# Kernel optimization log

Measured on AMD Instinct MI355X. Metric: run time of the kernel, lower is better.

Reference implementation:

```python
import jax, jax.numpy as jnp
import numpy as np

N = 50000
E = 800000
IN_DIM = 256
HID = 256
LAT = 64
H1 = 4
H2 = 4
O1 = HID // H1  # 64 per-head out of conv1
NEG_SLOPE = 0.2


def setup_inputs() -> dict:
    key = jax.random.key(0)
    ks = jax.random.split(key, 12)
    x = jax.random.normal(ks[0], (N, IN_DIM), dtype=jnp.float32)
    edge_index = jax.random.randint(ks[1], (2, E), 0, N, dtype=jnp.int64)
    g = lambda k, shape: jax.random.normal(k, shape, dtype=jnp.float32) * (1.0 / np.sqrt(shape[-1]))
    W1 = g(ks[2], (IN_DIM, H1 * O1))
    a_src1 = g(ks[3], (H1, O1))
    a_dst1 = g(ks[4], (H1, O1))
    b1 = jnp.zeros((H1 * O1,), dtype=jnp.float32)
    W2 = g(ks[5], (HID, H2 * LAT))
    a_src2 = g(ks[6], (H2, LAT))
    a_dst2 = g(ks[7], (H2, LAT))
    b2 = jnp.zeros((LAT,), dtype=jnp.float32)
    return {"x": x, "edge_index": edge_index, "W1": W1, "a_src1": a_src1,
            "a_dst1": a_dst1, "b1": b1, "W2": W2, "a_src2": a_src2,
            "a_dst2": a_dst2, "b2": b2}


def _gat_conv(x, src, dst, W, a_src, a_dst, bias, concat):
    # src/dst already include self-loops. x: (N, F_in)
    n, heads, out = x.shape[0], a_src.shape[0], a_src.shape[1]
    h = (x @ W).reshape(n, heads, out)                      # (N,H,O)
    al_src = jnp.einsum('nho,ho->nh', h, a_src)             # (N,H)
    al_dst = jnp.einsum('nho,ho->nh', h, a_dst)
    e = al_src[src] + al_dst[dst]                           # (Et,H)
    e = jnp.where(e > 0, e, NEG_SLOPE * e)                  # LeakyReLU(0.2)
    # softmax over incoming edges of each dst node
    m = jax.ops.segment_max(e, dst, num_segments=n)         # (N,H)
    p = jnp.exp(e - m[dst])
    denom = jax.ops.segment_sum(p, dst, num_segments=n)     # (N,H)
    alpha = p / denom[dst]                                  # (Et,H)
    msg = h[src] * alpha[:, :, None]                        # (Et,H,O)
    out_n = jax.ops.segment_sum(msg, dst, num_segments=n)   # (N,H,O)
    if concat:
        out_n = out_n.reshape(n, heads * out)
    else:
        out_n = out_n.mean(axis=1)
    return out_n + bias


def reference(x, edge_index, W1, a_src1, a_dst1, b1, W2, a_src2, a_dst2, b2):
    src, dst = edge_index[0], edge_index[1]
    # add self-loops (PyG GATConv default)
    loops = jnp.arange(N, dtype=edge_index.dtype)
    src_sl = jnp.concatenate([src, loops])
    dst_sl = jnp.concatenate([dst, loops])
    h = _gat_conv(x, src_sl, dst_sl, W1, a_src1, a_dst1, b1, concat=True)
    h = jax.nn.elu(h)
    z = _gat_conv(h, src_sl, dst_sl, W2, a_src2, a_dst2, b2, concat=False)
    # DotDecoder on original edge_index
    logits = jnp.einsum('ed,ed->e', z[src], z[dst])
    return logits
```

## Files before the change

kernel.cpp:

```cpp
#include <hip/hip_runtime.h>
#include <math.h>

#define N_NODES 50000
#define E_EDGES 800000
#define DIM 256
#define HEADS 4
#define HO 64
#define NEG_SLOPE 0.2f
#define SCAN_NBLK ((N_NODES + 255) / 256)

typedef __attribute__((ext_vector_type(8))) short bf16x8;
typedef __attribute__((ext_vector_type(4))) float f32x4;
typedef __attribute__((ext_vector_type(2))) float f32x2;

static __device__ inline ushort f2bf(float f) {
  union { float f; unsigned u; } v; v.f = f;
  unsigned r = (v.u + 0x7fff + ((v.u >> 16) & 1)) >> 16;
  return (ushort)r;
}
static __device__ inline float bf2f(ushort h) {
  union { unsigned u; float f; } v; v.u = ((unsigned)h) << 16;
  return v.f;
}

__global__ __launch_bounds__(256) void cvt_T2(const float* __restrict__ W1,
                                              const float* __restrict__ W2,
                                              ushort* __restrict__ bt1,
                                              ushort* __restrict__ bt2) {
  int gidx = blockIdx.x * 256 + threadIdx.x;
  const float* W = (gidx < DIM * DIM) ? W1 : W2;
  ushort* bt = (gidx < DIM * DIM) ? bt1 : bt2;
  int idx = gidx & (DIM * DIM - 1);
  int k = idx >> 8, n = idx & 255;
  bt[n * 256 + k] = f2bf(W[idx]);
}

#define GBM 128
#define GBK 32
#define LDK 40

template <bool AF32>
__global__ __launch_bounds__(256) void gemm_mfma(const void* __restrict__ Av,
                                                 const ushort* __restrict__ Bt,
                                                 ushort* __restrict__ Cbf, int M) {
  __shared__ __align__(16) ushort As[GBM][LDK];
  __shared__ __align__(16) ushort Bs[GBM][LDK];
  const int tid = threadIdx.x;
  const int lane = tid & 63;
  const int wave = tid >> 6;
  const int row0 = blockIdx.x * GBM;
  const int col0 = blockIdx.y * GBM;
  const int wm = (wave & 1) * 64;
  const int wn = (wave >> 1) * 64;
  const int rA = lane & 15;
  const int kb = (lane >> 4) * 8;

  f32x4 acc[4][4] = {};

  for (int k0 = 0; k0 < DIM; k0 += GBK) {
    if constexpr (AF32) {
      const float* A = (const float*)Av;
#pragma unroll
      for (int qq = 0; qq < 4; ++qq) {
        int q = tid + qq * 256;
        int r = q >> 3, c = q & 7;
        int grow = row0 + r;
        float4 v = make_float4(0.f, 0.f, 0.f, 0.f);
        if (grow < M) v = *(const float4*)&A[(size_t)grow * DIM + k0 + c * 4];
        ushort4 h;
        h.x = f2bf(v.x); h.y = f2bf(v.y); h.z = f2bf(v.z); h.w = f2bf(v.w);
        *(ushort4*)&As[r][c * 4] = h;
      }
    } else {
      const ushort* A = (const ushort*)Av;
#pragma unroll
      for (int qq = 0; qq < 2; ++qq) {
        int q = tid + qq * 256;
        int r = q >> 2, c = q & 3;
        int grow = row0 + r;
        bf16x8 v = {};
        if (grow < M) v = *(const bf16x8*)&A[(size_t)grow * DIM + k0 + c * 8];
        *(bf16x8*)&As[r][c * 8] = v;
      }
    }
#pragma unroll
    for (int qq = 0; qq < 2; ++qq) {
      int q = tid + qq * 256;
      int r = q >> 2, c = q & 3;
      *(bf16x8*)&Bs[r][c * 8] = *(const bf16x8*)&Bt[(size_t)(col0 + r) * DIM + k0 + c * 8];
    }
    __syncthreads();

    bf16x8 af[4], bfr[4];
#pragma unroll
    for (int mi = 0; mi < 4; ++mi) af[mi] = *(const bf16x8*)&As[wm + mi * 16 + rA][kb];
#pragma unroll
    for (int ni = 0; ni < 4; ++ni) bfr[ni] = *(const bf16x8*)&Bs[wn + ni * 16 + rA][kb];
#pragma unroll
    for (int mi = 0; mi < 4; ++mi)
#pragma unroll
      for (int ni = 0; ni < 4; ++ni)
        acc[mi][ni] = __builtin_amdgcn_mfma_f32_16x16x32_bf16(af[mi], bfr[ni], acc[mi][ni], 0, 0, 0);
    __syncthreads();
  }

#pragma unroll
  for (int mi = 0; mi < 4; ++mi) {
    int rbase = row0 + wm + mi * 16 + (lane >> 4) * 4;
#pragma unroll
    for (int ni = 0; ni < 4; ++ni) {
      int col = col0 + wn + ni * 16 + (lane & 15);
#pragma unroll
      for (int r = 0; r < 4; ++r) {
        int row = rbase + r;
        if (row < M) Cbf[(size_t)row * DIM + col] = f2bf(acc[mi][ni][r]);
      }
    }
  }
}

__global__ __launch_bounds__(256) void attn_logits(const ushort* __restrict__ h,
                                                   const float* __restrict__ a_src,
                                                   const float* __restrict__ a_dst,
                                                   float* __restrict__ al_s,
                                                   float* __restrict__ al_d) {
  int gid = blockIdx.x * blockDim.x + threadIdx.x;
  int node = gid >> 6;
  int lane = threadIdx.x & 63;
  if (node >= N_NODES) return;
  ushort4 hv = *(const ushort4*)&h[(size_t)node * DIM + lane * 4];
  float4 as = *(const float4*)&a_src[lane * 4];
  float4 ad = *(const float4*)&a_dst[lane * 4];
  float h0 = bf2f(hv.x), h1 = bf2f(hv.y), h2 = bf2f(hv.z), h3 = bf2f(hv.w);
  float s = h0 * as.x + h1 * as.y + h2 * as.z + h3 * as.w;
  float d = h0 * ad.x + h1 * ad.y + h2 * ad.z + h3 * ad.w;
#pragma unroll
  for (int off = 8; off >= 1; off >>= 1) {
    s += __shfl_xor(s, off, 64);
    d += __shfl_xor(d, off, 64);
  }
  if ((lane & 15) == 0) {
    int head = lane >> 4;
    al_s[node * HEADS + head] = s;
    al_d[node * HEADS + head] = d;
  }
}

__global__ __launch_bounds__(256) void histo(const int* __restrict__ dst, int* __restrict__ deg) {
  int e = blockIdx.x * blockDim.x + threadIdx.x;
  if (e < E_EDGES) atomicAdd(&deg[dst[e]], 1);
}

__global__ __launch_bounds__(256) void scan1(const int* __restrict__ deg,
                                             int* __restrict__ excl,
                                             int* __restrict__ blockSums) {
  __shared__ int tmp[256];
  int i = blockIdx.x * 256 + threadIdx.x;
  int v = (i < N_NODES) ? deg[i] : 0;
  tmp[threadIdx.x] = v;
  __syncthreads();
  for (int off = 1; off < 256; off <<= 1) {
    int t = (threadIdx.x >= off) ? tmp[threadIdx.x - off] : 0;
    __syncthreads();
    tmp[threadIdx.x] += t;
    __syncthreads();
  }
  int incl = tmp[threadIdx.x];
  if (i < N_NODES) excl[i] = incl - v;
  if (threadIdx.x == 255) blockSums[blockIdx.x] = incl;
}

__global__ __launch_bounds__(256) void scan2(int* __restrict__ blockSums) {
  __shared__ int tmp[256];
  int i = threadIdx.x;
  int v = (i < SCAN_NBLK) ? blockSums[i] : 0;
  tmp[i] = v;
  __syncthreads();
  for (int off = 1; off < 256; off <<= 1) {
    int t = (i >= off) ? tmp[i - off] : 0;
    __syncthreads();
    tmp[i] += t;
    __syncthreads();
  }
  if (i < SCAN_NBLK) blockSums[i] = tmp[i] - v;
}

__global__ __launch_bounds__(256) void scan3(int* __restrict__ excl,
                                             const int* __restrict__ blockSums,
                                             int* __restrict__ cursor) {
  int i = blockIdx.x * 256 + threadIdx.x;
  if (i < N_NODES) {
    int r = excl[i] + blockSums[blockIdx.x];
    excl[i] = r;
    cursor[i] = r;
  }
}

__global__ __launch_bounds__(256) void scatter(const int* __restrict__ src,
                                               const int* __restrict__ dst,
                                               int* __restrict__ cursor,
                                               int* __restrict__ csr_src) {
  int e = blockIdx.x * blockDim.x + threadIdx.x;
  if (e >= E_EDGES) return;
  int pos = atomicAdd(&cursor[dst[e]], 1);
  csr_src[pos] = src[e];
}

#define AGG_BODY(S)                                                         \
  {                                                                         \
    float e0 = als[(S) * HEADS + head] + aldv;                              \
    e0 = e0 > 0.f ? e0 : NEG_SLOPE * e0;                                    \
    float p = __expf(e0);                                                   \
    bf16x8 hv = *(const bf16x8*)&hbf[(size_t)(S) * DIM + c0];               \
    den += p;                                                               \
    const uint* uu = (const uint*)&hv;                                      \
    f32x2 pp = {p, p};                                                      \
    _Pragma("unroll")                                                       \
    for (int q = 0; q < 4; ++q) {                                           \
      f32x2 hh;                                                             \
      hh.x = __uint_as_float(uu[q] << 16);                                  \
      hh.y = __uint_as_float(uu[q] & 0xffff0000u);                          \
      acc2[q] += pp * hh;                                                   \
    }                                                                       \
  }

#define AGG_LOOP                                                            \
  int rs = rowptr[node];                                                    \
  int deg = ((node < N_NODES - 1) ? rowptr[node + 1] : E_EDGES) - rs;       \
  float aldv = ald[node * HEADS + head];                                    \
  float den = 0.f;                                                          \
  f32x2 acc2[4] = {};                                                       \
  int total = deg + 1;                                                      \
  int it = half;                                                            \
  for (; it + 4 < total; it += 6) {                                         \
    int s0 = csr_src[rs + it];                                              \
    int s1 = csr_src[rs + it + 2];                                          \
    int s2 = (it + 4 < deg) ? csr_src[rs + it + 4] : node;                  \
    AGG_BODY(s0)                                                            \
    AGG_BODY(s1)                                                            \
    AGG_BODY(s2)                                                            \
  }                                                                         \
  for (; it < total; it += 2) {                                             \
    int s0 = (it < deg) ? csr_src[rs + it] : node;                          \
    AGG_BODY(s0)                                                            \
  }                                                                         \
  den += __shfl_xor(den, 32, 64);                                           \
  float accs[8];                                                            \
  _Pragma("unroll")                                                         \
  for (int q = 0; q < 4; ++q) {                                             \
    accs[2 * q] = acc2[q].x + __shfl_xor(acc2[q].x, 32, 64);                \
    accs[2 * q + 1] = acc2[q].y + __shfl_xor(acc2[q].y, 32, 64);            \
  }

__global__ __launch_bounds__(256) void agg1(const int* __restrict__ rowptr,
                                            const int* __restrict__ csr_src,
                                            const ushort* __restrict__ hbf,
                                            const float* __restrict__ als,
                                            const float* __restrict__ ald,
                                            const float* __restrict__ bias,
                                            ushort* __restrict__ x2) {
  int gid = blockIdx.x * blockDim.x + threadIdx.x;
  int node = gid >> 6;
  if (node >= N_NODES) return;
  int lane = threadIdx.x & 63;
  int li = lane & 31, half = lane >> 5;
  int head = li >> 3;
  int c0 = li * 8;
  AGG_LOOP
  if (half == 0) {
    float inv = 1.f / den;
    ushort4 o0, o1;
    float r[8];
#pragma unroll
    for (int j = 0; j < 8; ++j) {
      r[j] = accs[j] * inv + bias[c0 + j];
      r[j] = r[j] > 0.f ? r[j] : expm1f(r[j]);
    }
    o0.x = f2bf(r[0]); o0.y = f2bf(r[1]); o0.z = f2bf(r[2]); o0.w = f2bf(r[3]);
    o1.x = f2bf(r[4]); o1.y = f2bf(r[5]); o1.z = f2bf(r[6]); o1.w = f2bf(r[7]);
    *(ushort4*)&x2[(size_t)node * DIM + c0] = o0;
    *(ushort4*)&x2[(size_t)node * DIM + c0 + 4] = o1;
  }
}

__global__ __launch_bounds__(256) void agg2(const int* __restrict__ rowptr,
                                            const int* __restrict__ csr_src,
                                            const ushort* __restrict__ hbf,
                                            const float* __restrict__ als,
                                            const float* __restrict__ ald,
                                            const float* __restrict__ b2,
                                            float* __restrict__ z) {
  int gid = blockIdx.x * blockDim.x + threadIdx.x;
  int node = gid >> 6;
  if (node >= N_NODES) return;
  int lane = threadIdx.x & 63;
  int li = lane & 31, half = lane >> 5;
  int head = li >> 3;
  int c0 = li * 8;
  AGG_LOOP
  float inv = 1.f / den;
  float r[8];
#pragma unroll
  for (int j = 0; j < 8; ++j) {
    r[j] = accs[j] * inv;
    r[j] += __shfl_xor(r[j], 8, 64);
    r[j] += __shfl_xor(r[j], 16, 64);
  }
  if (lane < 8) {
    int zc = li * 8;
    float4 v0 = make_float4(r[0] * 0.25f + b2[zc + 0], r[1] * 0.25f + b2[zc + 1],
                            r[2] * 0.25f + b2[zc + 2], r[3] * 0.25f + b2[zc + 3]);
    float4 v1 = make_float4(r[4] * 0.25f + b2[zc + 4], r[5] * 0.25f + b2[zc + 5],
                            r[6] * 0.25f + b2[zc + 6], r[7] * 0.25f + b2[zc + 7]);
    *(float4*)&z[(size_t)node * HO + zc] = v0;
    *(float4*)&z[(size_t)node * HO + zc + 4] = v1;
  }
}

__global__ __launch_bounds__(256) void decoder(const int* __restrict__ src,
                                               const int* __restrict__ dst,
                                               const float* __restrict__ z,
                                               float* __restrict__ out) {
  long long gid = (long long)blockIdx.x * blockDim.x + threadIdx.x;
  int e = (int)(gid >> 4);
  if (e >= E_EDGES) return;
  int l = threadIdx.x & 15;
  int s = src[e];
  int d = dst[e];
  float4 a = *(const float4*)&z[(size_t)s * HO + l * 4];
  float4 b = *(const float4*)&z[(size_t)d * HO + l * 4];
  float v = a.x * b.x + a.y * b.y + a.z * b.z + a.w * b.w;
#pragma unroll
  for (int off = 8; off >= 1; off >>= 1) v += __shfl_xor(v, off, 64);
  if (l == 0) out[e] = v;
}

extern "C" void kernel_launch(void* const* d_in, const int* in_sizes, int n_in,
                              void* d_out, int out_size, void* d_ws, size_t ws_size,
                              hipStream_t stream) {
  const float* x      = (const float*)d_in[0];
  const int*   ei     = (const int*)d_in[1];
  const float* W1     = (const float*)d_in[2];
  const float* a_src1 = (const float*)d_in[3];
  const float* a_dst1 = (const float*)d_in[4];
  const float* b1     = (const float*)d_in[5];
  const float* W2     = (const float*)d_in[6];
  const float* a_src2 = (const float*)d_in[7];
  const float* a_dst2 = (const float*)d_in[8];
  const float* b2     = (const float*)d_in[9];
  const int* src = ei;
  const int* dst = ei + E_EDGES;
  float* logits = (float*)d_out;

  float* zlat = (float*)d_ws;
  float* als1 = zlat + (size_t)N_NODES * HO;
  float* ald1 = als1 + N_NODES * HEADS;
  float* als2 = ald1 + N_NODES * HEADS;
  float* ald2 = als2 + N_NODES * HEADS;
  int* deg      = (int*)(ald2 + N_NODES * HEADS);
  int* rowptr   = deg + N_NODES;
  int* cursor   = rowptr + N_NODES;
  int* blockSums= cursor + N_NODES;
  int* csr_src  = blockSums + 256;
  ushort* hbf   = (ushort*)(csr_src + E_EDGES);
  ushort* x2bf  = hbf + (size_t)N_NODES * DIM;
  ushort* bt1   = x2bf + (size_t)N_NODES * DIM;
  ushort* bt2   = bt1 + DIM * DIM;

  dim3 blk(256);
  dim3 gemmGrid((N_NODES + GBM - 1) / GBM, DIM / GBM);
  int nodeBlocks = (N_NODES * 64 + 255) / 256;
  int edgeThreadBlocks = (E_EDGES + 255) / 256;
  int decBlocks  = (int)(((long long)E_EDGES * 16 + 255) / 256);

  hipMemsetAsync(deg, 0, N_NODES * sizeof(int), stream);
  hipLaunchKernelGGL(histo, dim3(edgeThreadBlocks), blk, 0, stream, dst, deg);
  hipLaunchKernelGGL(scan1, dim3(SCAN_NBLK), blk, 0, stream, deg, rowptr, blockSums);
  hipLaunchKernelGGL(scan2, dim3(1), blk, 0, stream, blockSums);
  hipLaunchKernelGGL(scan3, dim3(SCAN_NBLK), blk, 0, stream, rowptr, blockSums, cursor);
  hipLaunchKernelGGL(scatter, dim3(edgeThreadBlocks), blk, 0, stream, src, dst, cursor, csr_src);

  hipLaunchKernelGGL(cvt_T2, dim3(2 * DIM * DIM / 256), blk, 0, stream, W1, W2, bt1, bt2);

  gemm_mfma<true><<<gemmGrid, blk, 0, stream>>>((const void*)x, bt1, hbf, N_NODES);
  hipLaunchKernelGGL(attn_logits, dim3(nodeBlocks), blk, 0, stream, hbf, a_src1, a_dst1, als1, ald1);
  hipLaunchKernelGGL(agg1, dim3(nodeBlocks), blk, 0, stream, rowptr, csr_src, hbf, als1, ald1, b1, x2bf);

  gemm_mfma<false><<<gemmGrid, blk, 0, stream>>>((const void*)x2bf, bt2, hbf, N_NODES);
  hipLaunchKernelGGL(attn_logits, dim3(nodeBlocks), blk, 0, stream, hbf, a_src2, a_dst2, als2, ald2);
  hipLaunchKernelGGL(agg2, dim3(nodeBlocks), blk, 0, stream, rowptr, csr_src, hbf, als2, ald2, b2, zlat);

  hipLaunchKernelGGL(decoder, dim3(decBlocks), blk, 0, stream, src, dst, zlat, logits);
}
```

Baseline: 378.3 us.

## Fold attention logit projections into GEMM via precomputed W·a columns

Precomputes W·a_src and W·a_dst per head as extra bf16 weight rows, so the GEMM blocks in column tile zero compute the attention logits with extra MFMAs. This removes the two attn_logits kernels, which re-read the full bf16 h matrix. In exchange, the logits are now computed from bf16-rounded folded weights rather than from rounded h, which changes the rounding slightly. The blockIdx.y==0 blocks also carry extra MFMA work, which unbalances the GEMM grid a little.

```diff
diff --git a/kernel.cpp b/kernel.cpp
--- a/kernel.cpp
+++ b/kernel.cpp
@@ -8,6 +8,7 @@
 #define HO 64
 #define NEG_SLOPE 0.2f
 #define SCAN_NBLK ((N_NODES + 255) / 256)
+#define BT_ROWS 272
 
 typedef __attribute__((ext_vector_type(8))) short bf16x8;
 typedef __attribute__((ext_vector_type(4))) float f32x4;
@@ -23,16 +24,42 @@
   return v.f;
 }
 
-__global__ __launch_bounds__(256) void cvt_T2(const float* __restrict__ W1,
-                                              const float* __restrict__ W2,
-                                              ushort* __restrict__ bt1,
-                                              ushort* __restrict__ bt2) {
-  int gidx = blockIdx.x * 256 + threadIdx.x;
-  const float* W = (gidx < DIM * DIM) ? W1 : W2;
-  ushort* bt = (gidx < DIM * DIM) ? bt1 : bt2;
-  int idx = gidx & (DIM * DIM - 1);
-  int k = idx >> 8, n = idx & 255;
-  bt[n * 256 + k] = f2bf(W[idx]);
+__global__ __launch_bounds__(256) void prep_weights(const float* __restrict__ W1,
+                                                    const float* __restrict__ W2,
+                                                    const float* __restrict__ as1,
+                                                    const float* __restrict__ ad1,
+                                                    const float* __restrict__ as2,
+                                                    const float* __restrict__ ad2,
+                                                    ushort* __restrict__ bt1,
+                                                    ushort* __restrict__ bt2) {
+  int b = blockIdx.x;
+  int tid = threadIdx.x;
+  if (b < 512) {
+    const float* W = (b < 256) ? W1 : W2;
+    ushort* bt = (b < 256) ? bt1 : bt2;
+    int idx = ((b & 255) << 8) | tid;
+    int k = idx >> 8, n = idx & 255;
+    bt[n * 256 + k] = f2bf(W[idx]);
+  } else {
+    int k = tid;
+    for (int l = 0; l < 2; ++l) {
+      const float* W = l ? W2 : W1;
+      const float* as = l ? as2 : as1;
+      const float* ad = l ? ad2 : ad1;
+      ushort* bt = l ? bt2 : bt1;
+      for (int h = 0; h < HEADS; ++h) {
+        float s = 0.f, d = 0.f;
+        for (int o = 0; o < HO; ++o) {
+          float w = W[k * DIM + h * HO + o];
+          s += w * as[h * HO + o];
+          d += w * ad[h * HO + o];
+        }
+        bt[(256 + h) * 256 + k] = f2bf(s);
+        bt[(260 + h) * 256 + k] = f2bf(d);
+      }
+      for (int j = 0; j < 8; ++j) bt[(264 + j) * 256 + k] = 0;
+    }
+  }
 }
 
 #define GBM 128
@@ -42,9 +69,12 @@
 template <bool AF32>
 __global__ __launch_bounds__(256) void gemm_mfma(const void* __restrict__ Av,
                                                  const ushort* __restrict__ Bt,
-                                                 ushort* __restrict__ Cbf, int M) {
+                                                 ushort* __restrict__ Cbf,
+                                                 float* __restrict__ als,
+                                                 float* __restrict__ ald, int M) {
   __shared__ __align__(16) ushort As[GBM][LDK];
   __shared__ __align__(16) ushort Bs[GBM][LDK];
+  __shared__ __align__(16) ushort Es[16][LDK];
   const int tid = threadIdx.x;
   const int lane = tid & 63;
   const int wave = tid >> 6;
@@ -54,8 +84,10 @@
   const int wn = (wave >> 1) * 64;
   const int rA = lane & 15;
   const int kb = (lane >> 4) * 8;
+  const bool doE = (blockIdx.y == 0);
 
   f32x4 acc[4][4] = {};
+  f32x4 accE[4] = {};
 
   for (int k0 = 0; k0 < DIM; k0 += GBK) {
     if constexpr (AF32) {
@@ -89,6 +121,10 @@
       int r = q >> 2, c = q & 3;
       *(bf16x8*)&Bs[r][c * 8] = *(const bf16x8*)&Bt[(size_t)(col0 + r) * DIM + k0 + c * 8];
     }
+    if (doE && tid < 64) {
+      int r = tid >> 2, c = tid & 3;
+      *(bf16x8*)&Es[r][c * 8] = *(const bf16x8*)&Bt[(size_t)(256 + r) * DIM + k0 + c * 8];
+    }
     __syncthreads();
 
     bf16x8 af[4], bfr[4];
@@ -96,6 +132,12 @@
     for (int mi = 0; mi < 4; ++mi) af[mi] = *(const bf16x8*)&As[wm + mi * 16 + rA][kb];
 #pragma unroll
     for (int ni = 0; ni < 4; ++ni) bfr[ni] = *(const bf16x8*)&Bs[wn + ni * 16 + rA][kb];
+    if (doE && wn == 0) {
+      bf16x8 ef = *(const bf16x8*)&Es[rA][kb];
+#pragma unroll
+      for (int mi = 0; mi < 4; ++mi)
+        accE[mi] = __builtin_amdgcn_mfma_f32_16x16x32_bf16(af[mi], ef, accE[mi], 0, 0, 0);
+    }
 #pragma unroll
     for (int mi = 0; mi < 4; ++mi)
 #pragma unroll
@@ -117,32 +159,22 @@
       }
     }
   }
-}
-
-__global__ __launch_bounds__(256) void attn_logits(const ushort* __restrict__ h,
-                                                   const float* __restrict__ a_src,
-                                                   const float* __restrict__ a_dst,
-                                                   float* __restrict__ al_s,
-                                                   float* __restrict__ al_d) {
-  int gid = blockIdx.x * blockDim.x + threadIdx.x;
-  int node = gid >> 6;
-  int lane = threadIdx.x & 63;
-  if (node >= N_NODES) return;
-  ushort4 hv = *(const ushort4*)&h[(size_t)node * DIM + lane * 4];
-  float4 as = *(const float4*)&a_src[lane * 4];
-  float4 ad = *(const float4*)&a_dst[lane * 4];
-  float h0 = bf2f(hv.x), h1 = bf2f(hv.y), h2 = bf2f(hv.z), h3 = bf2f(hv.w);
-  float s = h0 * as.x + h1 * as.y + h2 * as.z + h3 * as.w;
-  float d = h0 * ad.x + h1 * ad.y + h2 * ad.z + h3 * ad.w;
-#pragma unroll
-  for (int off = 8; off >= 1; off >>= 1) {
-    s += __shfl_xor(s, off, 64);
-    d += __shfl_xor(d, off, 64);
-  }
-  if ((lane & 15) == 0) {
-    int head = lane >> 4;
-    al_s[node * HEADS + head] = s;
-    al_d[node * HEADS + head] = d;
+
+  if (doE && wn == 0) {
+    int col16 = lane & 15;
+#pragma unroll
+    for (int mi = 0; mi < 4; ++mi) {
+      int rbase = row0 + wm + mi * 16 + (lane >> 4) * 4;
+#pragma unroll
+      for (int r = 0; r < 4; ++r) {
+        int row = rbase + r;
+        if (row < M && col16 < 8) {
+          float v = accE[mi][r];
+          if (col16 < 4) als[row * HEADS + col16] = v;
+          else           ald[row * HEADS + (col16 - 4)] = v;
+        }
+      }
+    }
   }
 }
 
@@ -365,7 +397,7 @@
   ushort* hbf   = (ushort*)(csr_src + E_EDGES);
   ushort* x2bf  = hbf + (size_t)N_NODES * DIM;
   ushort* bt1   = x2bf + (size_t)N_NODES * DIM;
-  ushort* bt2   = bt1 + DIM * DIM;
+  ushort* bt2   = bt1 + BT_ROWS * DIM;
 
   dim3 blk(256);
   dim3 gemmGrid((N_NODES + GBM - 1) / GBM, DIM / GBM);
@@ -380,14 +412,13 @@
   hipLaunchKernelGGL(scan3, dim3(SCAN_NBLK), blk, 0, stream, rowptr, blockSums, cursor);
   hipLaunchKernelGGL(scatter, dim3(edgeThreadBlocks), blk, 0, stream, src, dst, cursor, csr_src);
 
-  hipLaunchKernelGGL(cvt_T2, dim3(2 * DIM * DIM / 256), blk, 0, stream, W1, W2, bt1, bt2);
-
-  gemm_mfma<true><<<gemmGrid, blk, 0, stream>>>((const void*)x, bt1, hbf, N_NODES);
-  hipLaunchKernelGGL(attn_logits, dim3(nodeBlocks), blk, 0, stream, hbf, a_src1, a_dst1, als1, ald1);
+  hipLaunchKernelGGL(prep_weights, dim3(513), blk, 0, stream,
+                     W1, W2, a_src1, a_dst1, a_src2, a_dst2, bt1, bt2);
+
+  gemm_mfma<true><<<gemmGrid, blk, 0, stream>>>((const void*)x, bt1, hbf, als1, ald1, N_NODES);
   hipLaunchKernelGGL(agg1, dim3(nodeBlocks), blk, 0, stream, rowptr, csr_src, hbf, als1, ald1, b1, x2bf);
 
-  gemm_mfma<false><<<gemmGrid, blk, 0, stream>>>((const void*)x2bf, bt2, hbf, N_NODES);
-  hipLaunchKernelGGL(attn_logits, dim3(nodeBlocks), blk, 0, stream, hbf, a_src2, a_dst2, als2, ald2);
+  gemm_mfma<false><<<gemmGrid, blk, 0, stream>>>((const void*)x2bf, bt2, hbf, als2, ald2, N_NODES);
   hipLaunchKernelGGL(agg2, dim3(nodeBlocks), blk, 0, stream, rowptr, csr_src, hbf, als2, ald2, b2, zlat);
 
   hipLaunchKernelGGL(decoder, dim3(decBlocks), blk, 0, stream, src, dst, zlat, logits);
```

After: 394.5 us. 1.04x slower.

## Run dot-product decoder over dst-sorted CSR to reuse destination embeddings

Applied to the files above, without the earlier changes.

The edge decoder now iterates per destination node over the CSR built for aggregation. Each node's z row is loaded once and reused for all incoming edges, and results are scattered to their original edge ids through a new csr_eid array written in the scatter kernel. This cuts random reads of z[dst] but adds an extra int write per edge in scatter and scattered output stores. It also adds load imbalance from varying degrees, with only 4 edges processed per wave iteration.

```diff
diff --git a/kernel.cpp b/kernel.cpp
--- a/kernel.cpp
+++ b/kernel.cpp
@@ -199,11 +199,13 @@
 __global__ __launch_bounds__(256) void scatter(const int* __restrict__ src,
                                                const int* __restrict__ dst,
                                                int* __restrict__ cursor,
-                                               int* __restrict__ csr_src) {
+                                               int* __restrict__ csr_src,
+                                               int* __restrict__ csr_eid) {
   int e = blockIdx.x * blockDim.x + threadIdx.x;
   if (e >= E_EDGES) return;
   int pos = atomicAdd(&cursor[dst[e]], 1);
   csr_src[pos] = src[e];
+  csr_eid[pos] = e;
 }
 
 #define AGG_BODY(S)                                                         \
@@ -317,22 +319,29 @@
   }
 }
 
-__global__ __launch_bounds__(256) void decoder(const int* __restrict__ src,
-                                               const int* __restrict__ dst,
-                                               const float* __restrict__ z,
-                                               float* __restrict__ out) {
-  long long gid = (long long)blockIdx.x * blockDim.x + threadIdx.x;
-  int e = (int)(gid >> 4);
-  if (e >= E_EDGES) return;
-  int l = threadIdx.x & 15;
-  int s = src[e];
-  int d = dst[e];
-  float4 a = *(const float4*)&z[(size_t)s * HO + l * 4];
-  float4 b = *(const float4*)&z[(size_t)d * HO + l * 4];
-  float v = a.x * b.x + a.y * b.y + a.z * b.z + a.w * b.w;
-#pragma unroll
-  for (int off = 8; off >= 1; off >>= 1) v += __shfl_xor(v, off, 64);
-  if (l == 0) out[e] = v;
+__global__ __launch_bounds__(256) void decoder_csr(const int* __restrict__ rowptr,
+                                                   const int* __restrict__ csr_src,
+                                                   const int* __restrict__ csr_eid,
+                                                   const float* __restrict__ z,
+                                                   float* __restrict__ out) {
+  int gid = blockIdx.x * blockDim.x + threadIdx.x;
+  int node = gid >> 6;
+  if (node >= N_NODES) return;
+  int lane = threadIdx.x & 63;
+  int g = lane >> 4, l = lane & 15;
+  int rs = rowptr[node];
+  int deg = ((node < N_NODES - 1) ? rowptr[node + 1] : E_EDGES) - rs;
+  if (deg == 0) return;
+  float4 zd = *(const float4*)&z[(size_t)node * HO + l * 4];
+  for (int it = g; it < deg; it += 4) {
+    int s = csr_src[rs + it];
+    int eid = csr_eid[rs + it];
+    float4 zs = *(const float4*)&z[(size_t)s * HO + l * 4];
+    float v = zs.x * zd.x + zs.y * zd.y + zs.z * zd.z + zs.w * zd.w;
+#pragma unroll
+    for (int off = 8; off >= 1; off >>= 1) v += __shfl_xor(v, off, 64);
+    if (l == 0) out[eid] = v;
+  }
 }
 
 extern "C" void kernel_launch(void* const* d_in, const int* in_sizes, int n_in,
@@ -362,7 +371,8 @@
   int* cursor   = rowptr + N_NODES;
   int* blockSums= cursor + N_NODES;
   int* csr_src  = blockSums + 256;
-  ushort* hbf   = (ushort*)(csr_src + E_EDGES);
+  int* csr_eid  = csr_src + E_EDGES;
+  ushort* hbf   = (ushort*)(csr_eid + E_EDGES);
   ushort* x2bf  = hbf + (size_t)N_NODES * DIM;
   ushort* bt1   = x2bf + (size_t)N_NODES * DIM;
   ushort* bt2   = bt1 + DIM * DIM;
@@ -371,14 +381,13 @@
   dim3 gemmGrid((N_NODES + GBM - 1) / GBM, DIM / GBM);
   int nodeBlocks = (N_NODES * 64 + 255) / 256;
   int edgeThreadBlocks = (E_EDGES + 255) / 256;
-  int decBlocks  = (int)(((long long)E_EDGES * 16 + 255) / 256);
 
   hipMemsetAsync(deg, 0, N_NODES * sizeof(int), stream);
   hipLaunchKernelGGL(histo, dim3(edgeThreadBlocks), blk, 0, stream, dst, deg);
   hipLaunchKernelGGL(scan1, dim3(SCAN_NBLK), blk, 0, stream, deg, rowptr, blockSums);
   hipLaunchKernelGGL(scan2, dim3(1), blk, 0, stream, blockSums);
   hipLaunchKernelGGL(scan3, dim3(SCAN_NBLK), blk, 0, stream, rowptr, blockSums, cursor);
-  hipLaunchKernelGGL(scatter, dim3(edgeThreadBlocks), blk, 0, stream, src, dst, cursor, csr_src);
+  hipLaunchKernelGGL(scatter, dim3(edgeThreadBlocks), blk, 0, stream, src, dst, cursor, csr_src, csr_eid);
 
   hipLaunchKernelGGL(cvt_T2, dim3(2 * DIM * DIM / 256), blk, 0, stream, W1, W2, bt1, bt2);
 
@@ -390,5 +399,5 @@
   hipLaunchKernelGGL(attn_logits, dim3(nodeBlocks), blk, 0, stream, hbf, a_src2, a_dst2, als2, ald2);
   hipLaunchKernelGGL(agg2, dim3(nodeBlocks), blk, 0, stream, rowptr, csr_src, hbf, als2, ald2, b2, zlat);
 
-  hipLaunchKernelGGL(decoder, dim3(decBlocks), blk, 0, stream, src, dst, zlat, logits);
-}
+  hipLaunchKernelGGL(decoder_csr, dim3(nodeBlocks), blk, 0, stream, rowptr, csr_src, csr_eid, zlat, logits);
+}
```

Result: no change. 382.3 us (+1.1%).

## Double-buffer LDS tiles in MFMA GEMM with register prefetch

Applied to the files above, without the earlier changes.

The GEMM main loop now prefetches the next K-tile of A and B from global memory into registers while MFMAs run on the current LDS buffer. The prefetched tile is then written into a second LDS buffer, which removes one barrier per iteration. This is meant to hide global load latency behind compute. In exchange it doubles LDS use and raises register pressure, which may lower occupancy.

```diff
diff --git a/kernel.cpp b/kernel.cpp
--- a/kernel.cpp
+++ b/kernel.cpp
@@ -38,13 +38,14 @@
 #define GBM 128
 #define GBK 32
 #define LDK 40
+#define NKT (DIM / GBK)
 
 template <bool AF32>
 __global__ __launch_bounds__(256) void gemm_mfma(const void* __restrict__ Av,
                                                  const ushort* __restrict__ Bt,
                                                  ushort* __restrict__ Cbf, int M) {
-  __shared__ __align__(16) ushort As[GBM][LDK];
-  __shared__ __align__(16) ushort Bs[GBM][LDK];
+  __shared__ __align__(16) ushort As[2][GBM][LDK];
+  __shared__ __align__(16) ushort Bs[2][GBM][LDK];
   const int tid = threadIdx.x;
   const int lane = tid & 63;
   const int wave = tid >> 6;
@@ -56,8 +57,11 @@
   const int kb = (lane >> 4) * 8;
 
   f32x4 acc[4][4] = {};
-
-  for (int k0 = 0; k0 < DIM; k0 += GBK) {
+  ushort4 a4[4];
+  bf16x8 a8[2];
+  bf16x8 b8[2];
+
+  auto loadA = [&](int k0) {
     if constexpr (AF32) {
       const float* A = (const float*)Av;
 #pragma unroll
@@ -69,7 +73,7 @@
         if (grow < M) v = *(const float4*)&A[(size_t)grow * DIM + k0 + c * 4];
         ushort4 h;
         h.x = f2bf(v.x); h.y = f2bf(v.y); h.z = f2bf(v.z); h.w = f2bf(v.w);
-        *(ushort4*)&As[r][c * 4] = h;
+        a4[qq] = h;
       }
     } else {
       const ushort* A = (const ushort*)Av;
@@ -80,28 +84,63 @@
         int grow = row0 + r;
         bf16x8 v = {};
         if (grow < M) v = *(const bf16x8*)&A[(size_t)grow * DIM + k0 + c * 8];
-        *(bf16x8*)&As[r][c * 8] = v;
+        a8[qq] = v;
       }
     }
+  };
+  auto loadB = [&](int k0) {
 #pragma unroll
     for (int qq = 0; qq < 2; ++qq) {
       int q = tid + qq * 256;
       int r = q >> 2, c = q & 3;
-      *(bf16x8*)&Bs[r][c * 8] = *(const bf16x8*)&Bt[(size_t)(col0 + r) * DIM + k0 + c * 8];
-    }
-    __syncthreads();
+      b8[qq] = *(const bf16x8*)&Bt[(size_t)(col0 + r) * DIM + k0 + c * 8];
+    }
+  };
+  auto writeLDS = [&](int buf) {
+    if constexpr (AF32) {
+#pragma unroll
+      for (int qq = 0; qq < 4; ++qq) {
+        int q = tid + qq * 256;
+        int r = q >> 3, c = q & 7;
+        *(ushort4*)&As[buf][r][c * 4] = a4[qq];
+      }
+    } else {
+#pragma unroll
+      for (int qq = 0; qq < 2; ++qq) {
+        int q = tid + qq * 256;
+        int r = q >> 2, c = q & 3;
+        *(bf16x8*)&As[buf][r][c * 8] = a8[qq];
+      }
+    }
+#pragma unroll
+    for (int qq = 0; qq < 2; ++qq) {
+      int q = tid + qq * 256;
+      int r = q >> 2, c = q & 3;
+      *(bf16x8*)&Bs[buf][r][c * 8] = b8[qq];
+    }
+  };
+
+  loadA(0); loadB(0); writeLDS(0);
+  __syncthreads();
+
+  int cur = 0;
+  for (int t = 0; t < NKT; ++t) {
+    if (t + 1 < NKT) { loadA((t + 1) * GBK); loadB((t + 1) * GBK); }
 
     bf16x8 af[4], bfr[4];
 #pragma unroll
-    for (int mi = 0; mi < 4; ++mi) af[mi] = *(const bf16x8*)&As[wm + mi * 16 + rA][kb];
-#pragma unroll
-    for (int ni = 0; ni < 4; ++ni) bfr[ni] = *(const bf16x8*)&Bs[wn + ni * 16 + rA][kb];
+    for (int mi = 0; mi < 4; ++mi) af[mi] = *(const bf16x8*)&As[cur][wm + mi * 16 + rA][kb];
+#pragma unroll
+    for (int ni = 0; ni < 4; ++ni) bfr[ni] = *(const bf16x8*)&Bs[cur][wn + ni * 16 + rA][kb];
 #pragma unroll
     for (int mi = 0; mi < 4; ++mi)
 #pragma unroll
       for (int ni = 0; ni < 4; ++ni)
         acc[mi][ni] = __builtin_amdgcn_mfma_f32_16x16x32_bf16(af[mi], bfr[ni], acc[mi][ni], 0, 0, 0);
+
+    if (t + 1 < NKT) writeLDS(cur ^ 1);
     __syncthreads();
+    cur ^= 1;
   }
 
 #pragma unroll
```

Result: faster. 366.7 us (-3.1%).
